# Performance work log

Measured on AMD Instinct MI355X. Metric: run time of the kernel, lower is better.

The kernel has to match this reference:

```python
import jax, jax.numpy as jnp
import numpy as np

NUM_EDGE_TYPES = 4
TIME_STEPS = (1, 1)  # one propagation step per layer, 2 layers
HIDDEN = 128
N_NODES = 50000
N_EDGES = 400000


def setup_inputs() -> dict:
    key = jax.random.key(0)
    ks = jax.random.split(key, 8)
    states = jax.random.normal(ks[0], (N_NODES, HIDDEN), jnp.float32)
    etype = jax.random.randint(ks[1], (N_EDGES,), 0, NUM_EDGE_TYPES, jnp.int32)
    src = jax.random.randint(ks[2], (N_EDGES,), 0, N_NODES, jnp.int32)
    dst = jax.random.randint(ks[3], (N_EDGES,), 0, N_NODES, jnp.int32)
    edges = jnp.stack([etype, src, dst], axis=-1)  # [E, 3] = (type, src, dst)
    L = len(TIME_STEPS)
    std = HIDDEN ** -0.5  # matches tf.random_normal_initializer(stddev=H**-0.5)
    type_W = jax.random.normal(ks[4], (L, NUM_EDGE_TYPES, HIDDEN, HIDDEN), jnp.float32) * std
    type_b = jax.random.normal(ks[5], (L, NUM_EDGE_TYPES, HIDDEN), jnp.float32) * std
    gru_kernel = jax.random.normal(ks[6], (L, HIDDEN, 3 * HIDDEN), jnp.float32) * std
    gru_rkernel = jax.random.normal(ks[7], (L, HIDDEN, 3 * HIDDEN), jnp.float32) * std
    gru_bias = jnp.zeros((L, 2, 3 * HIDDEN), jnp.float32)  # [input_bias, recurrent_bias]
    return dict(states=states, edges=edges, type_W=type_W, type_b=type_b,
                gru_kernel=gru_kernel, gru_rkernel=gru_rkernel, gru_bias=gru_bias)


def _gru_cell(x, h, kernel, rkernel, bias):
    # tf.keras.layers.GRUCell with defaults (reset_after=True, sigmoid/tanh)
    mx = x @ kernel + bias[0]   # [N, 3H]
    mh = h @ rkernel + bias[1]  # [N, 3H]
    xz, xr, xh = jnp.split(mx, 3, axis=-1)
    hz, hr, hh = jnp.split(mh, 3, axis=-1)
    z = jax.nn.sigmoid(xz + hz)
    r = jax.nn.sigmoid(xr + hr)
    c = jnp.tanh(xh + r * hh)
    return z * h + (1.0 - z) * c


def _propagate(h, layer_no, edges, type_W, type_b):
    etype, src, dst = edges[:, 0], edges[:, 1], edges[:, 2]
    src_states = h[src]  # [E, H] irregular gather
    msgs = jnp.zeros_like(src_states)
    # per-edge-type dense transform, combined via masking (jit-friendly
    # equivalent of tf.dynamic_partition + per-type matmul)
    for t in range(NUM_EDGE_TYPES):
        mt = src_states @ type_W[layer_no, t] + type_b[layer_no, t]
        msgs = msgs + jnp.where((etype == t)[:, None], mt, 0.0)
    # scatter-add messages into destination nodes
    return jax.ops.segment_sum(msgs, dst, num_segments=h.shape[0])


def reference(states, edges, type_W, type_b, gru_kernel, gru_rkernel, gru_bias):
    h = states
    for layer_no, steps in enumerate(TIME_STEPS):
        for _ in range(steps):
            agg = _propagate(h, layer_no, edges, type_W, type_b)
            h = _gru_cell(agg, h, gru_kernel[layer_no], gru_rkernel[layer_no], gru_bias[layer_no])
    return h
```

## Files before the change

### kernel.cpp

```cpp
#include <hip/hip_runtime.h>
#include <hip/hip_bf16.h>

#define H 128
#define NT 4
#define CAP4 40

typedef __attribute__((ext_vector_type(8))) _Float16 half8;
typedef __attribute__((ext_vector_type(8))) unsigned short ushort8;
typedef __attribute__((ext_vector_type(4))) float f32x4;

#if defined(__has_builtin)
#if __has_builtin(__builtin_amdgcn_global_load_lds)
#define HAS_GLL 1
#endif
#endif
#ifndef HAS_GLL
#define HAS_GLL 0
#endif

__device__ __forceinline__ float bf2f(unsigned short u) {
    union { unsigned int i; float f; } v;
    v.i = ((unsigned int)u) << 16;
    return v.f;
}

__device__ __forceinline__ unsigned short f2bf(float f) {
    union { float f; unsigned int i; } v;
    v.f = f;
    unsigned int x = v.i;
    unsigned int r = (x + 0x7fffu + ((x >> 16) & 1u)) >> 16;
    return (unsigned short)r;
}

__device__ __forceinline__ float fsigmoid(float x) {
    return 1.0f / (1.0f + __expf(-x));
}
__device__ __forceinline__ float ftanh(float x) {
    return 1.0f - 2.0f / (__expf(2.0f * x) + 1.0f);
}

__device__ __forceinline__ float readf(const void* p, long i, int isbf) {
    return isbf ? bf2f(((const unsigned short*)p)[i]) : ((const float*)p)[i];
}

__device__ __forceinline__ void gll16(const _Float16* g, _Float16* l) {
#if HAS_GLL
    __builtin_amdgcn_global_load_lds(
        (const __attribute__((address_space(1))) unsigned int*)g,
        (__attribute__((address_space(3))) unsigned int*)l, 16, 0, 0);
#else
    const int lane = threadIdx.x & 63;
    *(half8*)&l[lane * 8] = *(const half8*)g;
#endif
}

__device__ __forceinline__ half8 frag(const _Float16* lds, int r, int g) {
    return *(const half8*)&lds[r * 64 + ((g ^ (r & 7)) * 8)];
}

__global__ void detect_dtype(const unsigned short* __restrict__ states_u16,
                             int* __restrict__ flag) {
    __shared__ int cnt;
    if (threadIdx.x == 0) cnt = 0;
    __syncthreads();
    int local = 0;
    for (int i = threadIdx.x; i < 1024; i += 256) {
        unsigned short u = states_u16[2 * i];
        int e = (u >> 7) & 0xFF;
        if (e >= 96 && e <= 158) local++;
    }
    atomicAdd(&cnt, local);
    __syncthreads();
    if (threadIdx.x == 0) *flag = (cnt >= 512) ? 1 : 0;
}

__global__ void prep_all(
    const void* __restrict__ states, const void* __restrict__ type_W,
    const void* __restrict__ type_b, const void* __restrict__ gk,
    const void* __restrict__ gr, const void* __restrict__ grub,
    _Float16* __restrict__ h16, _Float16* __restrict__ BTw,
    _Float16* __restrict__ BTg, float* __restrict__ btab,
    float* __restrict__ gbsum, float* __restrict__ gb0c,
    float* __restrict__ gb1c, int* __restrict__ counts4,
    const int* __restrict__ flag,
    long NNH, int nBTw, int nBTg, int NC4, int LAYERS) {
    long i = (long)blockIdx.x * 256 + threadIdx.x;
    const int fl = *flag;
    if (i < NNH) {
        h16[i] = (_Float16)readf(states, i, fl);
        return;
    }
    i -= NNH;
    if (i < nBTw) {
        int l = (int)(i >> 16);
        int r16 = (int)(i & 65535);
        int cblk = r16 >> 13;
        int rem = r16 & 8191;
        int g = rem >> 7;
        int mm = (rem >> 3) & 15;
        int j = rem & 7;
        int c = cblk * 16 + mm;
        int k = g * 8 + j;
        int t = k >> 7, kk = k & 127;
        BTw[i] = (_Float16)readf(type_W, (((long)(l * NT + t) * H) + kk) * H + c, fl);
        return;
    }
    i -= nBTw;
    if (i < nBTg) {
        int l = (int)(i >> 17);
        int r17 = (int)(i & 131071);
        int ncblk = r17 >> 12;
        int rem = r17 & 4095;
        int g = rem >> 7;
        int mm = (rem >> 3) & 15;
        int j = rem & 7;
        int nc = ncblk * 16 + mm;
        int k = g * 8 + j;
        int gblk = nc >> 6, gate = (nc >> 4) & 3;
        int c = gblk * 16 + (nc & 15);
        float v = 0.0f;
        if (gate == 0) {
            v = (k < 128) ? readf(gk, ((long)l * H + k) * 384 + c, fl)
                          : readf(gr, ((long)l * H + (k - 128)) * 384 + c, fl);
        } else if (gate == 1) {
            v = (k < 128) ? readf(gk, ((long)l * H + k) * 384 + 128 + c, fl)
                          : readf(gr, ((long)l * H + (k - 128)) * 384 + 128 + c, fl);
        } else if (gate == 2) {
            if (k < 128) v = readf(gk, ((long)l * H + k) * 384 + 256 + c, fl);
        } else {
            if (k >= 128) v = readf(gr, ((long)l * H + (k - 128)) * 384 + 256 + c, fl);
        }
        BTg[i] = (_Float16)v;
        return;
    }
    i -= nBTg;
    if (i < NC4) {
        counts4[i] = 0;
        return;
    }
    i -= NC4;
    {
        int j = (int)i;
        if (j < LAYERS * NT * H) btab[j] = readf(type_b, j, fl);
        if (j < LAYERS * 256) {
            int l = j >> 8, c = j & 255;
            gbsum[j] = readf(grub, (long)l * 768 + c, fl) +
                       readf(grub, (long)l * 768 + 384 + c, fl);
        }
        if (j < LAYERS * H) {
            int l = j >> 7, c = j & 127;
            gb0c[j] = readf(grub, (long)l * 768 + 256 + c, fl);
            gb1c[j] = readf(grub, (long)l * 768 + 384 + 256 + c, fl);
        }
    }
}

__global__ void place_edges4(const int* __restrict__ edges, int* __restrict__ counts4,
                             int* __restrict__ buckets4, int NE) {
    int e = blockIdx.x * 256 + threadIdx.x;
    if (e >= NE) return;
    int t = edges[3 * e], src = edges[3 * e + 1], dst = edges[3 * e + 2];
    int slot = atomicAdd(&counts4[dst * 4 + t], 1);
    if (slot < CAP4) buckets4[((size_t)dst * 4 + t) * CAP4 + slot] = src;
}

__global__ __launch_bounds__(256) void gather4(
    const _Float16* __restrict__ h16, const int* __restrict__ counts4,
    const int* __restrict__ buckets4, _Float16* __restrict__ A4, int NN) {
    int node = blockIdx.x * 4 + (threadIdx.x >> 6);
    int lane = threadIdx.x & 63;
    int q = lane >> 4, i = lane & 15;
    if (node >= NN) return;
    int cnt = counts4[node * 4 + q];
    if (cnt > CAP4) cnt = CAP4;
    const int* bkt = buckets4 + ((size_t)node * 4 + q) * CAP4;

    float acc[8] = {};
    int e = 0;
    for (; e + 4 <= cnt; e += 4) {
        int s0 = bkt[e], s1 = bkt[e + 1], s2 = bkt[e + 2], s3 = bkt[e + 3];
        half8 v0 = *(const half8*)&h16[(size_t)s0 * H + i * 8];
        half8 v1 = *(const half8*)&h16[(size_t)s1 * H + i * 8];
        half8 v2 = *(const half8*)&h16[(size_t)s2 * H + i * 8];
        half8 v3 = *(const half8*)&h16[(size_t)s3 * H + i * 8];
#pragma unroll
        for (int j = 0; j < 8; j++)
            acc[j] += ((float)v0[j] + (float)v1[j]) + ((float)v2[j] + (float)v3[j]);
    }
    if (e + 2 <= cnt) {
        int s0 = bkt[e], s1 = bkt[e + 1];
        half8 v0 = *(const half8*)&h16[(size_t)s0 * H + i * 8];
        half8 v1 = *(const half8*)&h16[(size_t)s1 * H + i * 8];
#pragma unroll
        for (int j = 0; j < 8; j++) acc[j] += (float)v0[j] + (float)v1[j];
        e += 2;
    }
    if (e < cnt) {
        int s0 = bkt[e];
        half8 v0 = *(const half8*)&h16[(size_t)s0 * H + i * 8];
#pragma unroll
        for (int j = 0; j < 8; j++) acc[j] += (float)v0[j];
    }

    half8 o;
#pragma unroll
    for (int j = 0; j < 8; j++) o[j] = (_Float16)acc[j];
    *(half8*)&A4[((size_t)node * 4 + q) * H + i * 8] = o;
}

__global__ __launch_bounds__(256, 4) void layer_fused(
    const _Float16* __restrict__ A4,
    const _Float16* __restrict__ h16,
    const _Float16* __restrict__ BTw,
    const _Float16* __restrict__ BTg,
    const float* __restrict__ btab,
    const int4* __restrict__ cnt4,
    const float* __restrict__ gbsum,
    const float* __restrict__ gb0c,
    const float* __restrict__ gb1c,
    _Float16* __restrict__ hnext,
    void* __restrict__ outbuf,
    const int* __restrict__ flag, int NN) {
    __shared__ __align__(16) _Float16 As[2048];
    __shared__ __align__(16) _Float16 Bs[8192];
    __shared__ __align__(16) _Float16 aggL[4096];
    __shared__ __align__(16) _Float16 hL[4096];

    const int row0 = blockIdx.x * 32;
    const int tid = threadIdx.x;
    const int wave = tid >> 6, lane = tid & 63;
    const int m = lane & 15, quad = lane >> 4;

    f32x4 acc[2][2] = {};
    for (int kc = 0; kc < 8; kc++) {
        __syncthreads();
        {
            int R = wave * 8;
            int rl = R + (lane >> 3);
            int rg = row0 + rl;
            if (rg >= NN) rg = NN - 1;
            int chunk = (lane & 7) ^ (rl & 7);
            gll16(A4 + (size_t)rg * 512 + kc * 64 + chunk * 8, As + R * 64);
        }
#pragma unroll
        for (int r = 0; r < 4; r++) {
            int u = r * 256 + tid;
            int cblk = u >> 7, gp = (u >> 4) & 7, mm = u & 15;
            gll16(BTw + cblk * 8192 + (kc * 8 + gp) * 128 + mm * 8,
                  Bs + (r * 256 + wave * 64) * 8);
        }
        __syncthreads();
#pragma unroll
        for (int ks = 0; ks < 2; ks++) {
            half8 a[2], b[2];
#pragma unroll
            for (int mt = 0; mt < 2; mt++)
                a[mt] = frag(As, mt * 16 + m, ks * 4 + quad);
#pragma unroll
            for (int nt = 0; nt < 2; nt++)
                b[nt] = *(const half8*)&Bs[(wave * 2 + nt) * 1024 +
                                           (ks * 4 + quad) * 128 + m * 8];
#pragma unroll
            for (int mt = 0; mt < 2; mt++)
#pragma unroll
                for (int nt = 0; nt < 2; nt++)
                    acc[mt][nt] = __builtin_amdgcn_mfma_f32_16x16x32_f16(
                        a[mt], b[nt], acc[mt][nt], 0, 0, 0);
        }
    }

    {
        int R = wave * 8;
        int rl = R + (lane >> 3);
        int rg = row0 + rl;
        if (rg >= NN) rg = NN - 1;
        int chunk = (lane & 7) ^ (rl & 7);
        gll16(h16 + (size_t)rg * H + chunk * 8, hL + R * 64);
        gll16(h16 + (size_t)rg * H + 64 + chunk * 8, hL + 2048 + R * 64);
    }

#pragma unroll
    for (int mt = 0; mt < 2; mt++) {
#pragma unroll
        for (int i = 0; i < 4; i++) {
            int rl = mt * 16 + quad * 4 + i;
            int rg = row0 + rl;
            if (rg >= NN) rg = NN - 1;
            int4 c4 = cnt4[rg];
#pragma unroll
            for (int nt = 0; nt < 2; nt++) {
                int c = wave * 32 + nt * 16 + m;
                float bias = c4.x * btab[c] + c4.y * btab[128 + c] +
                             c4.z * btab[256 + c] + c4.w * btab[384 + c];
                int sub = c >> 6, cc = c & 63, g = cc >> 3;
                aggL[sub * 2048 + rl * 64 + ((g ^ (rl & 7)) * 8) + (cc & 7)] =
                    (_Float16)(acc[mt][nt][i] + bias);
            }
        }
    }
    __syncthreads();

    _Float16* hout16 = Bs;
    const int fl = outbuf ? *flag : 0;
    const int y = wave;
#pragma unroll
    for (int ch = 0; ch < 2; ch++) {
        f32x4 p[2][4] = {};
        const int ncb0 = y * 8 + ch * 4;
#pragma unroll
        for (int kc = 0; kc < 4; kc++) {
            const int ntA = (kc < 2) ? 2 : 3;
            const _Float16* Asrc = (kc < 2) ? (aggL + kc * 2048)
                                            : (hL + (kc - 2) * 2048);
#pragma unroll
            for (int ks = 0; ks < 2; ks++) {
                const int gk = kc * 8 + ks * 4 + quad;
                half8 a0 = frag(Asrc, m, ks * 4 + quad);
                half8 a1 = frag(Asrc, 16 + m, ks * 4 + quad);
                half8 b0 = *(const half8*)&BTg[(size_t)(ncb0 + 0) * 4096 +
                                               gk * 128 + m * 8];
                half8 b1 = *(const half8*)&BTg[(size_t)(ncb0 + 1) * 4096 +
                                               gk * 128 + m * 8];
                half8 b2 = *(const half8*)&BTg[(size_t)(ncb0 + ntA) * 4096 +
                                               gk * 128 + m * 8];
                p[0][0] = __builtin_amdgcn_mfma_f32_16x16x32_f16(a0, b0, p[0][0], 0, 0, 0);
                p[1][0] = __builtin_amdgcn_mfma_f32_16x16x32_f16(a1, b0, p[1][0], 0, 0, 0);
                p[0][1] = __builtin_amdgcn_mfma_f32_16x16x32_f16(a0, b1, p[0][1], 0, 0, 0);
                p[1][1] = __builtin_amdgcn_mfma_f32_16x16x32_f16(a1, b1, p[1][1], 0, 0, 0);
                p[0][ntA] = __builtin_amdgcn_mfma_f32_16x16x32_f16(a0, b2, p[0][ntA], 0, 0, 0);
                p[1][ntA] = __builtin_amdgcn_mfma_f32_16x16x32_f16(a1, b2, p[1][ntA], 0, 0, 0);
            }
        }

        const int c = (2 * y + ch) * 16 + m;
        const float bz = gbsum[c];
        const float br = gbsum[128 + c];
        const float bx = gb0c[c];
        const float bh = gb1c[c];
        const int sub = c >> 6, cc = c & 63, hg = cc >> 3, hj = cc & 7;
#pragma unroll
        for (int mt = 0; mt < 2; mt++) {
#pragma unroll
            for (int i = 0; i < 4; i++) {
                int rl = mt * 16 + quad * 4 + i;
                int row = row0 + rl;
                float z = fsigmoid(p[mt][0][i] + bz);
                float r = fsigmoid(p[mt][1][i] + br);
                float ccand =
                    ftanh((p[mt][2][i] + bx) + r * (p[mt][3][i] + bh));
                float hv = (float)hL[sub * 2048 + rl * 64 +
                                     ((hg ^ (rl & 7)) * 8) + hj];
                float hn = z * hv + (1.0f - z) * ccand;
                if (outbuf) {
                    if (row < NN) {
                        size_t oi = (size_t)row * H + c;
                        if (fl) ((unsigned short*)outbuf)[oi] = f2bf(hn);
                        else    ((float*)outbuf)[oi] = hn;
                    }
                } else {
                    hout16[rl * 136 + c] = (_Float16)hn;
                }
            }
        }
    }

    if (!outbuf) {
        __syncthreads();
        int r = tid >> 3, s = tid & 7;
        int row = row0 + r;
        if (row < NN) {
            half8 v0 = *(const half8*)&hout16[r * 136 + s * 16];
            half8 v1 = *(const half8*)&hout16[r * 136 + s * 16 + 8];
            size_t o = (size_t)row * H + s * 16;
            *(half8*)&hnext[o] = v0;
            *(half8*)&hnext[o + 8] = v1;
        }
    }
}

extern "C" void kernel_launch(void* const* d_in, const int* in_sizes, int n_in,
                              void* d_out, int out_size, void* d_ws, size_t ws_size,
                              hipStream_t stream) {
    const void* states = d_in[0];
    const int*  edges  = (const int*)d_in[1];
    const void* type_W = d_in[2];
    const void* type_b = d_in[3];
    const void* gruk   = d_in[4];
    const void* grur   = d_in[5];
    const void* grub   = d_in[6];

    const int NN = in_sizes[0] / H;
    const int NE = in_sizes[1] / 3;
    const int nW = in_sizes[2];
    const int LAYERS = nW / (NT * H * H);

    char* w = (char*)d_ws;
    int* flag = (int*)w;                               w += 64;
    _Float16* h16A  = (_Float16*)w;                    w += (size_t)NN * H * 2;
    _Float16* h16B  = (_Float16*)w;                    w += (size_t)NN * H * 2;
    _Float16* A4    = (_Float16*)w;                    w += (size_t)NN * 4 * H * 2;
    _Float16* BTw = (_Float16*)w;                      w += (size_t)LAYERS * H * 512 * 2;
    _Float16* BTg = (_Float16*)w;                      w += (size_t)LAYERS * 512 * 256 * 2;
    float* btab  = (float*)w;                          w += (size_t)LAYERS * NT * H * 4;
    float* gbsum = (float*)w;                          w += (size_t)LAYERS * 256 * 4;
    float* gb0c  = (float*)w;                          w += (size_t)LAYERS * H * 4;
    float* gb1c  = (float*)w;                          w += (size_t)LAYERS * H * 4;
    int* counts4 = (int*)w;                            w += (size_t)NN * 4 * 4;
    int* buckets4 = (int*)w;

    detect_dtype<<<1, 256, 0, stream>>>((const unsigned short*)states, flag);

    const long NNH = (long)NN * H;
    const int nBTw = LAYERS * 65536;
    const int nBTg = LAYERS * 131072;
    const int NC4 = NN * 4;
    const long ptotal = NNH + nBTw + nBTg + NC4 + LAYERS * NT * H;
    prep_all<<<(int)((ptotal + 255) / 256), 256, 0, stream>>>(
        states, type_W, type_b, gruk, grur, grub,
        h16A, BTw, BTg, btab, gbsum, gb0c, gb1c, counts4, flag,
        NNH, nBTw, nBTg, NC4, LAYERS);

    place_edges4<<<(NE + 255) / 256, 256, 0, stream>>>(edges, counts4, buckets4, NE);

    const int rt32 = (NN + 31) / 32;
    for (int L = 0; L < LAYERS; L++) {
        const _Float16* hcur = (L & 1) ? h16B : h16A;
        _Float16* hnext      = (L & 1) ? h16A : h16B;

        gather4<<<(NN + 3) / 4, 256, 0, stream>>>(hcur, counts4, buckets4, A4, NN);

        layer_fused<<<rt32, 256, 0, stream>>>(
            A4, hcur,
            BTw + (size_t)L * H * 512,
            BTg + (size_t)L * 512 * 256,
            btab + (size_t)L * NT * H, (const int4*)counts4,
            gbsum + (size_t)L * 256, gb0c + (size_t)L * H, gb1c + (size_t)L * H,
            hnext, (L == LAYERS - 1) ? d_out : nullptr, flag, NN);
    }
}
```

Before: 261.3 us.

## Preload full A tile into LDS and read type weights directly from global

The message-transform GEMM now loads all eight K-chunks of the A4 rows into a larger shared buffer in one go, with a single barrier, instead of reloading A and B chunks each iteration with two barriers. The B operand (per-type weights) is read directly from global/cache as half8 fragments rather than staged through LDS. This removes per-iteration barriers and LDS staging of weights. In exchange it uses more shared memory, lowers the launch-bounds occupancy hint from 4 to 3, and relies on cached global reads for B.

Result: no change. 261.3 us (-0.0%).

```diff
diff --git a/kernel.cpp b/kernel.cpp
--- a/kernel.cpp
+++ b/kernel.cpp
@@ -208,7 +208,7 @@
     *(half8*)&A4[((size_t)node * 4 + q) * H + i * 8] = o;
 }
 
-__global__ __launch_bounds__(256, 4) void layer_fused(
+__global__ __launch_bounds__(256, 3) void layer_fused(
     const _Float16* __restrict__ A4,
     const _Float16* __restrict__ h16,
     const _Float16* __restrict__ BTw,
@@ -221,8 +221,7 @@
     _Float16* __restrict__ hnext,
     void* __restrict__ outbuf,
     const int* __restrict__ flag, int NN) {
-    __shared__ __align__(16) _Float16 As[2048];
-    __shared__ __align__(16) _Float16 Bs[8192];
+    __shared__ __align__(16) _Float16 As[16384];
     __shared__ __align__(16) _Float16 aggL[4096];
     __shared__ __align__(16) _Float16 hL[4096];
 
@@ -230,44 +229,6 @@
     const int tid = threadIdx.x;
     const int wave = tid >> 6, lane = tid & 63;
     const int m = lane & 15, quad = lane >> 4;
-
-    f32x4 acc[2][2] = {};
-    for (int kc = 0; kc < 8; kc++) {
-        __syncthreads();
-        {
-            int R = wave * 8;
-            int rl = R + (lane >> 3);
-            int rg = row0 + rl;
-            if (rg >= NN) rg = NN - 1;
-            int chunk = (lane & 7) ^ (rl & 7);
-            gll16(A4 + (size_t)rg * 512 + kc * 64 + chunk * 8, As + R * 64);
-        }
-#pragma unroll
-        for (int r = 0; r < 4; r++) {
-            int u = r * 256 + tid;
-            int cblk = u >> 7, gp = (u >> 4) & 7, mm = u & 15;
-            gll16(BTw + cblk * 8192 + (kc * 8 + gp) * 128 + mm * 8,
-                  Bs + (r * 256 + wave * 64) * 8);
-        }
-        __syncthreads();
-#pragma unroll
-        for (int ks = 0; ks < 2; ks++) {
-            half8 a[2], b[2];
-#pragma unroll
-            for (int mt = 0; mt < 2; mt++)
-                a[mt] = frag(As, mt * 16 + m, ks * 4 + quad);
-#pragma unroll
-            for (int nt = 0; nt < 2; nt++)
-                b[nt] = *(const half8*)&Bs[(wave * 2 + nt) * 1024 +
-                                           (ks * 4 + quad) * 128 + m * 8];
-#pragma unroll
-            for (int mt = 0; mt < 2; mt++)
-#pragma unroll
-                for (int nt = 0; nt < 2; nt++)
-                    acc[mt][nt] = __builtin_amdgcn_mfma_f32_16x16x32_f16(
-                        a[mt], b[nt], acc[mt][nt], 0, 0, 0);
-        }
-    }
 
     {
         int R = wave * 8;
@@ -275,8 +236,33 @@
         int rg = row0 + rl;
         if (rg >= NN) rg = NN - 1;
         int chunk = (lane & 7) ^ (rl & 7);
+        const _Float16* arow = A4 + (size_t)rg * 512 + chunk * 8;
+#pragma unroll
+        for (int kc = 0; kc < 8; kc++)
+            gll16(arow + kc * 64, As + kc * 2048 + R * 64);
         gll16(h16 + (size_t)rg * H + chunk * 8, hL + R * 64);
         gll16(h16 + (size_t)rg * H + 64 + chunk * 8, hL + 2048 + R * 64);
+    }
+    __syncthreads();
+
+    f32x4 acc[2][2] = {};
+#pragma unroll
+    for (int kc = 0; kc < 8; kc++) {
+        const _Float16* Ak = As + kc * 2048;
+#pragma unroll
+        for (int ks = 0; ks < 2; ks++) {
+            const int gk = kc * 8 + ks * 4 + quad;
+            half8 a0 = frag(Ak, m, ks * 4 + quad);
+            half8 a1 = frag(Ak, 16 + m, ks * 4 + quad);
+            half8 b0 = *(const half8*)&BTw[(size_t)(wave * 2 + 0) * 8192 +
+                                           gk * 128 + m * 8];
+            half8 b1 = *(const half8*)&BTw[(size_t)(wave * 2 + 1) * 8192 +
+                                           gk * 128 + m * 8];
+            acc[0][0] = __builtin_amdgcn_mfma_f32_16x16x32_f16(a0, b0, acc[0][0], 0, 0, 0);
+            acc[1][0] = __builtin_amdgcn_mfma_f32_16x16x32_f16(a1, b0, acc[1][0], 0, 0, 0);
+            acc[0][1] = __builtin_amdgcn_mfma_f32_16x16x32_f16(a0, b1, acc[0][1], 0, 0, 0);
+            acc[1][1] = __builtin_amdgcn_mfma_f32_16x16x32_f16(a1, b1, acc[1][1], 0, 0, 0);
+        }
     }
 
 #pragma unroll
@@ -300,7 +286,7 @@
     }
     __syncthreads();
 
-    _Float16* hout16 = Bs;
+    _Float16* hout16 = As;
     const int fl = outbuf ? *flag : 0;
     const int y = wave;
 #pragma unroll
```

## Transform node states per edge type before gathering instead of after

Applied to the files above, without the earlier changes.

Rather than gathering raw source states into per-type sums and then multiplying by the type weights, the code first computes Y_t = h·W_t for all nodes and types with a new MFMA kernel. It then gathers and sums the transformed rows across types, adding the count-weighted bias, and feeds a slimmer GRU kernel. This drops the K=512 message GEMM from the fused kernel and shrinks the gather output to one row per node. In exchange it writes and reads a 4×N×H fp16 Y tensor and adds a third kernel launch per layer.

Measured after the change: 408.6 us. 56.4% more time.

```diff
diff --git a/kernel.cpp b/kernel.cpp
--- a/kernel.cpp
+++ b/kernel.cpp
@@ -78,12 +78,12 @@
     const void* __restrict__ states, const void* __restrict__ type_W,
     const void* __restrict__ type_b, const void* __restrict__ gk,
     const void* __restrict__ gr, const void* __restrict__ grub,
-    _Float16* __restrict__ h16, _Float16* __restrict__ BTw,
+    _Float16* __restrict__ h16, _Float16* __restrict__ BTy,
     _Float16* __restrict__ BTg, float* __restrict__ btab,
     float* __restrict__ gbsum, float* __restrict__ gb0c,
     float* __restrict__ gb1c, int* __restrict__ counts4,
     const int* __restrict__ flag,
-    long NNH, int nBTw, int nBTg, int NC4, int LAYERS) {
+    long NNH, int nBTy, int nBTg, int NC4, int LAYERS) {
     long i = (long)blockIdx.x * 256 + threadIdx.x;
     const int fl = *flag;
     if (i < NNH) {
@@ -91,21 +91,21 @@
         return;
     }
     i -= NNH;
-    if (i < nBTw) {
+    if (i < nBTy) {
         int l = (int)(i >> 16);
         int r16 = (int)(i & 65535);
-        int cblk = r16 >> 13;
-        int rem = r16 & 8191;
+        int ncblk = r16 >> 11;
+        int rem = r16 & 2047;
         int g = rem >> 7;
         int mm = (rem >> 3) & 15;
         int j = rem & 7;
-        int c = cblk * 16 + mm;
+        int nc = ncblk * 16 + mm;
+        int t = nc >> 7, c = nc & 127;
         int k = g * 8 + j;
-        int t = k >> 7, kk = k & 127;
-        BTw[i] = (_Float16)readf(type_W, (((long)(l * NT + t) * H) + kk) * H + c, fl);
+        BTy[i] = (_Float16)readf(type_W, (((long)(l * NT + t) * H) + k) * H + c, fl);
         return;
     }
-    i -= nBTw;
+    i -= nBTy;
     if (i < nBTg) {
         int l = (int)(i >> 17);
         int r17 = (int)(i & 131071);
@@ -164,9 +164,74 @@
     if (slot < CAP4) buckets4[((size_t)dst * 4 + t) * CAP4 + slot] = src;
 }
 
-__global__ __launch_bounds__(256) void gather4(
-    const _Float16* __restrict__ h16, const int* __restrict__ counts4,
-    const int* __restrict__ buckets4, _Float16* __restrict__ A4, int NN) {
+__global__ __launch_bounds__(256, 3) void ygemm(
+    const _Float16* __restrict__ h16,
+    const _Float16* __restrict__ BTy,
+    _Float16* __restrict__ Y,
+    int NN) {
+    __shared__ __align__(16) _Float16 hT[4096];
+    __shared__ __align__(16) _Float16 Ybuf[4 * 4352];
+
+    const int row0 = blockIdx.x * 32;
+    const int tid = threadIdx.x;
+    const int wave = tid >> 6, lane = tid & 63;
+    const int m = lane & 15, quad = lane >> 4;
+
+    {
+        int R = wave * 8;
+        int rl = R + (lane >> 3);
+        int rg = row0 + rl;
+        if (rg >= NN) rg = NN - 1;
+        int chunk = (lane & 7) ^ (rl & 7);
+        gll16(h16 + (size_t)rg * H + chunk * 8, hT + R * 64);
+        gll16(h16 + (size_t)rg * H + 64 + chunk * 8, hT + 2048 + R * 64);
+    }
+    __syncthreads();
+
+    f32x4 acc[2][8] = {};
+#pragma unroll
+    for (int ks = 0; ks < 4; ks++) {
+        const int gk = ks * 4 + quad;
+        const _Float16* hsub = hT + (gk >> 3) * 2048;
+        half8 a0 = frag(hsub, m, gk & 7);
+        half8 a1 = frag(hsub, 16 + m, gk & 7);
+#pragma unroll
+        for (int nt = 0; nt < 8; nt++) {
+            const int ncb = wave * 8 + nt;
+            half8 b = *(const half8*)&BTy[((size_t)ncb << 11) + gk * 128 + m * 8];
+            acc[0][nt] = __builtin_amdgcn_mfma_f32_16x16x32_f16(a0, b, acc[0][nt], 0, 0, 0);
+            acc[1][nt] = __builtin_amdgcn_mfma_f32_16x16x32_f16(a1, b, acc[1][nt], 0, 0, 0);
+        }
+    }
+
+    _Float16* yb = Ybuf + wave * 4352;
+#pragma unroll
+    for (int mt = 0; mt < 2; mt++)
+#pragma unroll
+        for (int nt = 0; nt < 8; nt++)
+#pragma unroll
+            for (int i = 0; i < 4; i++) {
+                int rl = mt * 16 + quad * 4 + i;
+                yb[rl * 136 + nt * 16 + m] = (_Float16)acc[mt][nt][i];
+            }
+
+    {
+        int r = lane >> 1, s = lane & 1;
+        int row = row0 + r;
+        if (row < NN) {
+            _Float16* dst = Y + ((size_t)wave * NN + row) * H + s * 64;
+            const _Float16* src = yb + r * 136 + s * 64;
+#pragma unroll
+            for (int k = 0; k < 8; k++)
+                *(half8*)&dst[k * 8] = *(const half8*)&src[k * 8];
+        }
+    }
+}
+
+__global__ __launch_bounds__(256) void gatherY(
+    const _Float16* __restrict__ Y, const int* __restrict__ counts4,
+    const int* __restrict__ buckets4, const float* __restrict__ btab,
+    _Float16* __restrict__ agg16, int NN) {
     int node = blockIdx.x * 4 + (threadIdx.x >> 6);
     int lane = threadIdx.x & 63;
     int q = lane >> 4, i = lane & 15;
@@ -174,100 +239,73 @@
     int cnt = counts4[node * 4 + q];
     if (cnt > CAP4) cnt = CAP4;
     const int* bkt = buckets4 + ((size_t)node * 4 + q) * CAP4;
+    const _Float16* Yq = Y + (size_t)q * NN * H;
 
     float acc[8] = {};
     int e = 0;
     for (; e + 4 <= cnt; e += 4) {
         int s0 = bkt[e], s1 = bkt[e + 1], s2 = bkt[e + 2], s3 = bkt[e + 3];
-        half8 v0 = *(const half8*)&h16[(size_t)s0 * H + i * 8];
-        half8 v1 = *(const half8*)&h16[(size_t)s1 * H + i * 8];
-        half8 v2 = *(const half8*)&h16[(size_t)s2 * H + i * 8];
-        half8 v3 = *(const half8*)&h16[(size_t)s3 * H + i * 8];
+        half8 v0 = *(const half8*)&Yq[(size_t)s0 * H + i * 8];
+        half8 v1 = *(const half8*)&Yq[(size_t)s1 * H + i * 8];
+        half8 v2 = *(const half8*)&Yq[(size_t)s2 * H + i * 8];
+        half8 v3 = *(const half8*)&Yq[(size_t)s3 * H + i * 8];
 #pragma unroll
         for (int j = 0; j < 8; j++)
             acc[j] += ((float)v0[j] + (float)v1[j]) + ((float)v2[j] + (float)v3[j]);
     }
     if (e + 2 <= cnt) {
         int s0 = bkt[e], s1 = bkt[e + 1];
-        half8 v0 = *(const half8*)&h16[(size_t)s0 * H + i * 8];
-        half8 v1 = *(const half8*)&h16[(size_t)s1 * H + i * 8];
+        half8 v0 = *(const half8*)&Yq[(size_t)s0 * H + i * 8];
+        half8 v1 = *(const half8*)&Yq[(size_t)s1 * H + i * 8];
 #pragma unroll
         for (int j = 0; j < 8; j++) acc[j] += (float)v0[j] + (float)v1[j];
         e += 2;
     }
     if (e < cnt) {
         int s0 = bkt[e];
-        half8 v0 = *(const half8*)&h16[(size_t)s0 * H + i * 8];
+        half8 v0 = *(const half8*)&Yq[(size_t)s0 * H + i * 8];
 #pragma unroll
         for (int j = 0; j < 8; j++) acc[j] += (float)v0[j];
     }
 
-    half8 o;
-#pragma unroll
-    for (int j = 0; j < 8; j++) o[j] = (_Float16)acc[j];
-    *(half8*)&A4[((size_t)node * 4 + q) * H + i * 8] = o;
-}
-
-__global__ __launch_bounds__(256, 4) void layer_fused(
-    const _Float16* __restrict__ A4,
+#pragma unroll
+    for (int j = 0; j < 8; j++) {
+        acc[j] += __shfl_xor(acc[j], 16, 64);
+        acc[j] += __shfl_xor(acc[j], 32, 64);
+    }
+
+    if (q == 0) {
+        int4 c4 = *(const int4*)&counts4[node * 4];
+        half8 o;
+#pragma unroll
+        for (int j = 0; j < 8; j++) {
+            int col = i * 8 + j;
+            float b = c4.x * btab[col] + c4.y * btab[128 + col] +
+                      c4.z * btab[256 + col] + c4.w * btab[384 + col];
+            o[j] = (_Float16)(acc[j] + b);
+        }
+        *(half8*)&agg16[(size_t)node * H + i * 8] = o;
+    }
+}
+
+__global__ __launch_bounds__(256, 6) void gru_fused(
+    const _Float16* __restrict__ agg16,
     const _Float16* __restrict__ h16,
-    const _Float16* __restrict__ BTw,
     const _Float16* __restrict__ BTg,
-    const float* __restrict__ btab,
-    const int4* __restrict__ cnt4,
     const float* __restrict__ gbsum,
     const float* __restrict__ gb0c,
     const float* __restrict__ gb1c,
     _Float16* __restrict__ hnext,
     void* __restrict__ outbuf,
     const int* __restrict__ flag, int NN) {
-    __shared__ __align__(16) _Float16 As[2048];
-    __shared__ __align__(16) _Float16 Bs[8192];
     __shared__ __align__(16) _Float16 aggL[4096];
     __shared__ __align__(16) _Float16 hL[4096];
+    __shared__ __align__(16) _Float16 hout16[4352];
 
     const int row0 = blockIdx.x * 32;
     const int tid = threadIdx.x;
     const int wave = tid >> 6, lane = tid & 63;
     const int m = lane & 15, quad = lane >> 4;
-
-    f32x4 acc[2][2] = {};
-    for (int kc = 0; kc < 8; kc++) {
-        __syncthreads();
-        {
-            int R = wave * 8;
-            int rl = R + (lane >> 3);
-            int rg = row0 + rl;
-            if (rg >= NN) rg = NN - 1;
-            int chunk = (lane & 7) ^ (rl & 7);
-            gll16(A4 + (size_t)rg * 512 + kc * 64 + chunk * 8, As + R * 64);
-        }
-#pragma unroll
-        for (int r = 0; r < 4; r++) {
-            int u = r * 256 + tid;
-            int cblk = u >> 7, gp = (u >> 4) & 7, mm = u & 15;
-            gll16(BTw + cblk * 8192 + (kc * 8 + gp) * 128 + mm * 8,
-                  Bs + (r * 256 + wave * 64) * 8);
-        }
-        __syncthreads();
-#pragma unroll
-        for (int ks = 0; ks < 2; ks++) {
-            half8 a[2], b[2];
-#pragma unroll
-            for (int mt = 0; mt < 2; mt++)
-                a[mt] = frag(As, mt * 16 + m, ks * 4 + quad);
-#pragma unroll
-            for (int nt = 0; nt < 2; nt++)
-                b[nt] = *(const half8*)&Bs[(wave * 2 + nt) * 1024 +
-                                           (ks * 4 + quad) * 128 + m * 8];
-#pragma unroll
-            for (int mt = 0; mt < 2; mt++)
-#pragma unroll
-                for (int nt = 0; nt < 2; nt++)
-                    acc[mt][nt] = __builtin_amdgcn_mfma_f32_16x16x32_f16(
-                        a[mt], b[nt], acc[mt][nt], 0, 0, 0);
-        }
-    }
 
     {
         int R = wave * 8;
@@ -275,32 +313,13 @@
         int rg = row0 + rl;
         if (rg >= NN) rg = NN - 1;
         int chunk = (lane & 7) ^ (rl & 7);
+        gll16(agg16 + (size_t)rg * H + chunk * 8, aggL + R * 64);
+        gll16(agg16 + (size_t)rg * H + 64 + chunk * 8, aggL + 2048 + R * 64);
         gll16(h16 + (size_t)rg * H + chunk * 8, hL + R * 64);
         gll16(h16 + (size_t)rg * H + 64 + chunk * 8, hL + 2048 + R * 64);
     }
-
-#pragma unroll
-    for (int mt = 0; mt < 2; mt++) {
-#pragma unroll
-        for (int i = 0; i < 4; i++) {
-            int rl = mt * 16 + quad * 4 + i;
-            int rg = row0 + rl;
-            if (rg >= NN) rg = NN - 1;
-            int4 c4 = cnt4[rg];
-#pragma unroll
-            for (int nt = 0; nt < 2; nt++) {
-                int c = wave * 32 + nt * 16 + m;
-                float bias = c4.x * btab[c] + c4.y * btab[128 + c] +
-                             c4.z * btab[256 + c] + c4.w * btab[384 + c];
-                int sub = c >> 6, cc = c & 63, g = cc >> 3;
-                aggL[sub * 2048 + rl * 64 + ((g ^ (rl & 7)) * 8) + (cc & 7)] =
-                    (_Float16)(acc[mt][nt][i] + bias);
-            }
-        }
-    }
     __syncthreads();
 
-    _Float16* hout16 = Bs;
     const int fl = outbuf ? *flag : 0;
     const int y = wave;
 #pragma unroll
@@ -398,8 +417,9 @@
     int* flag = (int*)w;                               w += 64;
     _Float16* h16A  = (_Float16*)w;                    w += (size_t)NN * H * 2;
     _Float16* h16B  = (_Float16*)w;                    w += (size_t)NN * H * 2;
-    _Float16* A4    = (_Float16*)w;                    w += (size_t)NN * 4 * H * 2;
-    _Float16* BTw = (_Float16*)w;                      w += (size_t)LAYERS * H * 512 * 2;
+    _Float16* Y     = (_Float16*)w;                    w += (size_t)NN * 4 * H * 2;
+    _Float16* agg16 = (_Float16*)w;                    w += (size_t)NN * H * 2;
+    _Float16* BTy = (_Float16*)w;                      w += (size_t)LAYERS * H * 512 * 2;
     _Float16* BTg = (_Float16*)w;                      w += (size_t)LAYERS * 512 * 256 * 2;
     float* btab  = (float*)w;                          w += (size_t)LAYERS * NT * H * 4;
     float* gbsum = (float*)w;                          w += (size_t)LAYERS * 256 * 4;
@@ -411,14 +431,14 @@
     detect_dtype<<<1, 256, 0, stream>>>((const unsigned short*)states, flag);
 
     const long NNH = (long)NN * H;
-    const int nBTw = LAYERS * 65536;
+    const int nBTy = LAYERS * 65536;
     const int nBTg = LAYERS * 131072;
     const int NC4 = NN * 4;
-    const long ptotal = NNH + nBTw + nBTg + NC4 + LAYERS * NT * H;
+    const long ptotal = NNH + nBTy + nBTg + NC4 + LAYERS * NT * H;
     prep_all<<<(int)((ptotal + 255) / 256), 256, 0, stream>>>(
         states, type_W, type_b, gruk, grur, grub,
-        h16A, BTw, BTg, btab, gbsum, gb0c, gb1c, counts4, flag,
-        NNH, nBTw, nBTg, NC4, LAYERS);
+        h16A, BTy, BTg, btab, gbsum, gb0c, gb1c, counts4, flag,
+        NNH, nBTy, nBTg, NC4, LAYERS);
 
     place_edges4<<<(NE + 255) / 256, 256, 0, stream>>>(edges, counts4, buckets4, NE);
 
@@ -427,13 +447,15 @@
         const _Float16* hcur = (L & 1) ? h16B : h16A;
         _Float16* hnext      = (L & 1) ? h16A : h16B;
 
-        gather4<<<(NN + 3) / 4, 256, 0, stream>>>(hcur, counts4, buckets4, A4, NN);
-
-        layer_fused<<<rt32, 256, 0, stream>>>(
-            A4, hcur,
-            BTw + (size_t)L * H * 512,
+        ygemm<<<rt32, 256, 0, stream>>>(
+            hcur, BTy + (size_t)L * H * 512, Y, NN);
+
+        gatherY<<<(NN + 3) / 4, 256, 0, stream>>>(
+            Y, counts4, buckets4, btab + (size_t)L * NT * H, agg16, NN);
+
+        gru_fused<<<rt32, 256, 0, stream>>>(
+            agg16, hcur,
             BTg + (size_t)L * 512 * 256,
-            btab + (size_t)L * NT * H, (const int4*)counts4,
             gbsum + (size_t)L * 256, gb0c + (size_t)L * H, gb1c + (size_t)L * H,
             hnext, (L == LAYERS - 1) ? d_out : nullptr, flag, NN);
     }
```
